# Performance work log

Hardware: AMD Instinct MI355X
Metric: run time of the kernel (lower is better)

The kernel has to match this reference:

```python
import jax, jax.numpy as jnp
import numpy as np

N = 1024      # codeword length (input_size == output_size)
H1 = 3072     # edges of Tanner graph 1
H2 = 4096     # edges of Tanner graph 2
D1 = 6        # per-row mask degree, graph 1
D2 = 8        # per-row mask degree, graph 2
B = 2048      # batch
CLIP = 0.999999


def _row_indices(rng, rows, cols, deg):
    # deg distinct column indices per row (nonzeros of the binary CN mask)
    u = rng.random((rows, cols))
    return np.argsort(u, axis=1)[:, :deg].astype(np.int32)


def setup_inputs() -> dict:
    key = jax.random.key(0)
    ks = jax.random.split(key, 12)
    rng = np.random.default_rng(0)
    x = jax.random.normal(ks[0], (B, N), dtype=jnp.float32) * 2.0
    # CN-update masks as index lists
    idx1_first = jnp.asarray(_row_indices(rng, H1, N, D1))
    idx1_mid = jnp.asarray(_row_indices(rng, H1, H1, D1))
    idx2_first = jnp.asarray(_row_indices(rng, H2, N, D2))
    idx2_mid = jnp.asarray(_row_indices(rng, H2, H2, D2))
    # VN-update weights: xavier-like init pre-multiplied by sparse binary mask
    def sparse_w(k, shape, p):
        k1, k2 = jax.random.split(k)
        w = jax.random.normal(k1, shape, dtype=jnp.float32) * (1.0 / np.sqrt(shape[1]))
        m = (jax.random.uniform(k2, shape) < p).astype(jnp.float32)
        return w * m
    Wv1 = jnp.stack([sparse_w(jax.random.fold_in(ks[1], i), (H1, H1), 0.01) for i in range(5)])
    Wout1 = jnp.stack([sparse_w(jax.random.fold_in(ks[2], i), (N, H1), 0.01) for i in range(5)])
    Wv2 = jnp.stack([sparse_w(jax.random.fold_in(ks[3], i), (H2, H2), 0.01) for i in range(5)])
    Wout2 = jnp.stack([sparse_w(jax.random.fold_in(ks[4], i), (N, H2), 0.01) for i in range(5)])
    # bias scaling vectors: init eye(N) in the torch module; small perturbation to avoid triviality
    S = jnp.stack([jnp.eye(N, dtype=jnp.float32)
                   + 0.01 * jax.random.normal(jax.random.fold_in(ks[5], i), (N, N), dtype=jnp.float32)
                   for i in range(10)])
    B1 = jax.random.normal(ks[6], (N, H1), dtype=jnp.float32) * 0.02
    B2 = jax.random.normal(ks[7], (N, H2), dtype=jnp.float32) * 0.02
    return {"x": x, "S": S, "B1": B1, "B2": B2,
            "Wv1": Wv1, "Wout1": Wout1, "Wv2": Wv2, "Wout2": Wout2,
            "idx1_first": idx1_first, "idx1_mid": idx1_mid,
            "idx2_first": idx2_first, "idx2_mid": idx2_mid}


def cn_update(x, idx):
    # x: (B, in), idx: (out, deg) -> (B, out)
    vals = x[:, idx]                                   # (B, out, deg) gather
    nz = vals != 0.0
    prod = jnp.prod(jnp.where(nz, vals, 1.0), axis=-1)  # zeros act as 1
    return jnp.where(jnp.any(nz, axis=-1), prod, 0.0)   # all-zero rows -> 0


def reference(x, S, B1, B2, Wv1, Wout1, Wv2, Wout2,
              idx1_first, idx1_mid, idx2_first, idx2_mid):
    llrs = []
    for k in range(10):  # 10 unrolled BP iterations, alternating the two graphs
        g1 = (k % 2 == 0)
        j = k // 2
        Bm = B1 if g1 else B2
        Wv = Wv1[j] if g1 else Wv2[j]
        Wo = Wout1[j] if g1 else Wout2[j]
        idf = idx1_first if g1 else idx2_first
        idm = idx1_mid if g1 else idx2_mid
        chS = x @ S[k]                                  # Channel_LLR @ bias_scaling
        t = jnp.tanh(0.5 * x)
        t = jnp.clip(cn_update(t, idf), -CLIP, CLIP)
        t = 2.0 * jnp.arctanh(t)
        t = jnp.tanh(0.5 * (t @ Wv.T + chS @ Bm))
        t = jnp.clip(cn_update(t, idm), -CLIP, CLIP)
        t = 2.0 * jnp.arctanh(t)
        x = t @ Wo.T + chS
        llrs.append(jax.nn.sigmoid(x))
    return tuple(llrs)
```

## Files before the change

kernel.cpp:

```cpp
#include <hip/hip_runtime.h>
#include <hip/hip_bf16.h>
#include <stdint.h>
#include <stddef.h>

using bf16 = __hip_bfloat16;
typedef __attribute__((ext_vector_type(8))) short short8;
typedef __attribute__((ext_vector_type(2))) float f32x2;
typedef __attribute__((ext_vector_type(4))) float f32x4;
typedef __attribute__((ext_vector_type(4))) unsigned u32x4;

constexpr int BATCH = 2048;
constexpr int NN    = 1024;
constexpr int H1C   = 3072;
constexpr int H2C   = 4096;
constexpr int CAP   = 128;

constexpr int ROW_WV1 = 0;
constexpr int ROW_WO1 = 5 * H1C;
constexpr int ROW_WV2 = ROW_WO1 + 5 * NN;
constexpr int ROW_WO2 = ROW_WV2 + 5 * H2C;
constexpr int ROWS_TOTAL = ROW_WO2 + 5 * NN;

__device__ __forceinline__ unsigned short f2bf(float f) {
  unsigned u = __float_as_uint(f);
  unsigned r = 0x7FFFu + ((u >> 16) & 1u);
  return (unsigned short)((u + r) >> 16);
}
__device__ __forceinline__ float bf2f(short s) {
  return __uint_as_float(((unsigned)(unsigned short)s) << 16);
}

__device__ __forceinline__ unsigned short phi_enc(float x) {
  const float e = expf(-fabsf(x));
  const float phi = logf((1.f + e) / (1.f - e));
  return (unsigned short)(f2bf(phi) | (unsigned short)((__float_as_uint(x) >> 31) << 15));
}

__device__ __forceinline__ void gload16(const void* g, void* lds_base) {
  __builtin_amdgcn_global_load_lds(
      (const __attribute__((address_space(1))) void*)g,
      (__attribute__((address_space(3))) void*)lds_base, 16, 0, 0);
}

template<int D>
__device__ __forceinline__ void cn_math(const short8* v, float* rs) {
  float s[8];
  unsigned sg[8];
  bool any[8];
#pragma unroll
  for (int e = 0; e < 8; ++e) { s[e] = 0.f; sg[e] = 0u; any[e] = false; }
#pragma unroll
  for (int d = 0; d < D; ++d) {
#pragma unroll
    for (int e = 0; e < 8; ++e) {
      const unsigned bits = (unsigned)(unsigned short)v[d][e];
      sg[e] ^= bits >> 15;
      const unsigned a = bits & 0x7FFFu;
      const bool nz = (a != 0x7F80u);
      any[e] |= nz;
      s[e] += nz ? __uint_as_float(a << 16) : 0.f;
    }
  }
#pragma unroll
  for (int e = 0; e < 8; ++e) {
    const float y = fmaxf(s[e], 1.0000005e-6f);
    const float u = expf(-y);
    float r = logf((1.f + u) / (1.f - u));
    r = any[e] ? r : 0.f;
    rs[e] = __uint_as_float(__float_as_uint(r) | (sg[e] << 31));
  }
}

__device__ __forceinline__ void cn_store_fp8(const float* rs, uint8_t* dst) {
  int lo = 0, hi = 0;
  lo = __builtin_amdgcn_cvt_pk_fp8_f32(rs[0], rs[1], lo, false);
  lo = __builtin_amdgcn_cvt_pk_fp8_f32(rs[2], rs[3], lo, true);
  hi = __builtin_amdgcn_cvt_pk_fp8_f32(rs[4], rs[5], hi, false);
  hi = __builtin_amdgcn_cvt_pk_fp8_f32(rs[6], rs[7], hi, true);
  int2 o; o.x = lo; o.y = hi;
  *(int2*)dst = o;
}

__global__ __launch_bounds__(256, 2) void gemm_bt(
    const bf16* __restrict__ A, const bf16* __restrict__ BT,
    float* __restrict__ C, bf16* __restrict__ Cb, const float* __restrict__ add,
    int M, int Nd, int K)
{
  __shared__ bf16 As[128 * 32];
  __shared__ bf16 Bs[128 * 32];
  const int tid  = threadIdx.x;
  const int lane = tid & 63;
  const int w    = tid >> 6;
  const int bn = blockIdx.x, bm = blockIdx.y;
  const int wm = (w >> 1) * 64, wn = (w & 1) * 64;
  const int l15 = lane & 15;
  const int lk  = (lane >> 4) * 8;
  const int ld4 = (lane >> 4) * 4;
  const int sr  = lane >> 2;
  const int kc  = (lane & 3) * 8;

  f32x4 acc[4][4];
#pragma unroll
  for (int i = 0; i < 4; ++i)
#pragma unroll
    for (int j = 0; j < 4; ++j)
#pragma unroll
      for (int e = 0; e < 4; ++e) acc[i][j][e] = 0.f;

  const size_t rA = (size_t)bm * 128;
  const size_t rB = (size_t)bn * 128;

  for (int kt = 0; kt < K; kt += 32) {
#pragma unroll
    for (int c = 0; c < 2; ++c) {
      const int slot = w * 2 + c;
      const int r = slot * 16 + sr;
      gload16(A  + (rA + r) * (size_t)K + kt + kc, &As[slot * 512]);
      gload16(BT + (rB + r) * (size_t)K + kt + kc, &Bs[slot * 512]);
    }
    __syncthreads();
    short8 af[4], bfr[4];
#pragma unroll
    for (int f = 0; f < 4; ++f) {
      af[f]  = *(const short8*)&As[(wm + f * 16 + l15) * 32 + lk];
      bfr[f] = *(const short8*)&Bs[(wn + f * 16 + l15) * 32 + lk];
    }
#pragma unroll
    for (int i = 0; i < 4; ++i)
#pragma unroll
      for (int j = 0; j < 4; ++j)
        acc[i][j] = __builtin_amdgcn_mfma_f32_16x16x32_bf16(af[i], bfr[j], acc[i][j], 0, 0, 0);
    __syncthreads();
  }

#pragma unroll
  for (int i = 0; i < 4; ++i) {
    const int row0 = bm * 128 + wm + i * 16 + ld4;
#pragma unroll
    for (int j = 0; j < 4; ++j) {
      const int col = bn * 128 + wn + j * 16 + l15;
#pragma unroll
      for (int e = 0; e < 4; ++e) {
        const size_t o = (size_t)(row0 + e) * Nd + col;
        float v = acc[i][j][e];
        if (add) v += add[o];
        if (C)  C[o] = v;
        if (Cb) Cb[o] = __float2bfloat16(v);
      }
    }
  }
}

template<int D>
__global__ __launch_bounds__(256, 2) void zgemm_cn(
    const bf16* __restrict__ A, const bf16* __restrict__ BT, bf16* __restrict__ Cb,
    int K, int gb,
    const unsigned short* __restrict__ src, const int* __restrict__ idx,
    uint8_t* __restrict__ outf8)
{
  __shared__ bf16 As[128 * 32];
  __shared__ bf16 Bs[128 * 32];
  const int bid = blockIdx.x;
  if (bid < gb) {
    const int tid  = threadIdx.x;
    const int lane = tid & 63;
    const int w    = tid >> 6;
    const int bn = bid & 15;
    const int bm = bid >> 4;
    const int wm = (w >> 1) * 64, wn = (w & 1) * 64;
    const int l15 = lane & 15;
    const int lk  = (lane >> 4) * 8;
    const int ld4 = (lane >> 4) * 4;
    const int sr  = lane >> 2;
    const int kc  = (lane & 3) * 8;

    f32x4 acc[4][4];
#pragma unroll
    for (int i = 0; i < 4; ++i)
#pragma unroll
      for (int j = 0; j < 4; ++j)
#pragma unroll
        for (int e = 0; e < 4; ++e) acc[i][j][e] = 0.f;

    const size_t rA = (size_t)bm * 128;
    const size_t rB = (size_t)bn * 128;

    for (int kt = 0; kt < K; kt += 32) {
#pragma unroll
      for (int c = 0; c < 2; ++c) {
        const int slot = w * 2 + c;
        const int r = slot * 16 + sr;
        gload16(A  + (rA + r) * (size_t)K + kt + kc, &As[slot * 512]);
        gload16(BT + (rB + r) * (size_t)K + kt + kc, &Bs[slot * 512]);
      }
      __syncthreads();
      short8 af[4], bfr[4];
#pragma unroll
      for (int f = 0; f < 4; ++f) {
        af[f]  = *(const short8*)&As[(wm + f * 16 + l15) * 32 + lk];
        bfr[f] = *(const short8*)&Bs[(wn + f * 16 + l15) * 32 + lk];
      }
#pragma unroll
      for (int i = 0; i < 4; ++i)
#pragma unroll
        for (int j = 0; j < 4; ++j)
          acc[i][j] = __builtin_amdgcn_mfma_f32_16x16x32_bf16(af[i], bfr[j], acc[i][j], 0, 0, 0);
      __syncthreads();
    }

#pragma unroll
    for (int i = 0; i < 4; ++i) {
      const int row0 = bm * 128 + wm + i * 16 + ld4;
#pragma unroll
      for (int j = 0; j < 4; ++j) {
        const int col = bn * 128 + wn + j * 16 + l15;
#pragma unroll
        for (int e = 0; e < 4; ++e)
          Cb[(size_t)(row0 + e) * BATCH + col] = __float2bfloat16(acc[i][j][e]);
      }
    }
  } else {
    const int h = bid - gb;
    const int b = threadIdx.x * 8;
    const int* ir = idx + (size_t)h * D;
    int rows[D];
#pragma unroll
    for (int d = 0; d < D; ++d) rows[d] = ir[d];
    short8 v[D];
#pragma unroll
    for (int d = 0; d < D; ++d)
      v[d] = *(const short8*)(src + (size_t)rows[d] * BATCH + b);
    float rs[8];
    cn_math<D>(v, rs);
    cn_store_fp8(rs, outf8 + (size_t)h * BATCH + b);
  }
}

__global__ __launch_bounds__(256) void prep_smit(const float* __restrict__ S, bf16* __restrict__ out)
{
  __shared__ float ls[64][65];
  const int k = blockIdx.z;
  const int n0 = blockIdx.x * 64, m0 = blockIdx.y * 64;
  const float* Sk = S + (size_t)k * NN * NN;
  bf16* ok = out + (size_t)k * NN * NN;
  const int tc = threadIdx.x & 63, tr = threadIdx.x >> 6;
#pragma unroll
  for (int i = 0; i < 16; ++i) {
    const int r = tr + i * 4;
    ls[r][tc] = Sk[(size_t)(m0 + r) * NN + n0 + tc];
  }
  __syncthreads();
#pragma unroll
  for (int i = 0; i < 16; ++i) {
    const int r = tr + i * 4;
    float v = ls[tc][r] - ((m0 + tc) == (n0 + r) ? 1.f : 0.f);
    ok[(size_t)(n0 + r) * NN + m0 + tc] = __float2bfloat16(v);
  }
}

__global__ __launch_bounds__(256) void prep_bt(const float* __restrict__ Bsrc, bf16* __restrict__ out, int H)
{
  __shared__ float ls[64][65];
  const int h0 = blockIdx.x * 64, n0 = blockIdx.y * 64;
  const int tc = threadIdx.x & 63, tr = threadIdx.x >> 6;
#pragma unroll
  for (int i = 0; i < 16; ++i) {
    const int r = tr + i * 4;
    ls[r][tc] = Bsrc[(size_t)(n0 + r) * H + h0 + tc];
  }
  __syncthreads();
#pragma unroll
  for (int i = 0; i < 16; ++i) {
    const int r = tr + i * 4;
    out[(size_t)(h0 + r) * NN + n0 + tc] = __float2bfloat16(ls[tc][r]);
  }
}

__global__ __launch_bounds__(256) void csr_build(
    const float* __restrict__ W, int rowlen,
    unsigned* __restrict__ pack, int* __restrict__ nnz, int row_off)
{
  const int row = blockIdx.x;
  const float* wr = W + (size_t)row * rowlen;
  const size_t base = (size_t)(row_off + row) * CAP;
  __shared__ int wtot[4];
  __shared__ int cbase;
  if (threadIdx.x == 0) cbase = 0;
  __syncthreads();
  const int lane = threadIdx.x & 63, wv = threadIdx.x >> 6;
  for (int c0 = 0; c0 < rowlen; c0 += 256) {
    const int c = c0 + threadIdx.x;
    const float v = wr[c];
    const bool nz = (v != 0.f);
    const unsigned long long m = __ballot(nz);
    const int rank = __popcll(m & ((1ull << lane) - 1ull));
    if (lane == 0) wtot[wv] = __popcll(m);
    __syncthreads();
    int pre = cbase;
    for (int i = 0; i < wv; ++i) pre += wtot[i];
    if (nz) {
      const int p = pre + rank;
      if (p < CAP) pack[base + p] = ((unsigned)f2bf(v) << 16) | (unsigned)c;
    }
    __syncthreads();
    if (threadIdx.x == 0) cbase += wtot[0] + wtot[1] + wtot[2] + wtot[3];
    __syncthreads();
  }
  if (threadIdx.x == 0) nnz[row_off + row] = (cbase < CAP ? cbase : CAP);
}

template<int D>
__global__ __launch_bounds__(256) void cn_kernel(
    const unsigned short* __restrict__ src,
    const int* __restrict__ idx,
    uint8_t* __restrict__ out)
{
  const int h = blockIdx.x;
  const int b = threadIdx.x * 8;
  const int* ir = idx + (size_t)h * D;
  int rows[D];
#pragma unroll
  for (int d = 0; d < D; ++d) rows[d] = ir[d];
  short8 v[D];
#pragma unroll
  for (int d = 0; d < D; ++d)
    v[d] = *(const short8*)(src + (size_t)rows[d] * BATCH + b);
  float rs[8];
  cn_math<D>(v, rs);
  cn_store_fp8(rs, out + (size_t)h * BATCH + b);
}

__global__ __launch_bounds__(256) void sparse_wv(
    const unsigned short* __restrict__ zb, const uint8_t* __restrict__ t1f8,
    const unsigned* __restrict__ pack, const int* __restrict__ nnz,
    int rowoff, unsigned short* __restrict__ t2p)
{
  const int h = blockIdx.x;
  const int b = threadIdx.x * 8;
  const int rg = rowoff + h;
  const unsigned* pr = pack + (size_t)rg * CAP;
  const int n = nnz[rg];
  const short8 z = *(const short8*)(zb + (size_t)h * BATCH + b);
  f32x4 a0, a1;
#pragma unroll
  for (int e = 0; e < 4; ++e) { a0[e] = bf2f(z[e]); a1[e] = bf2f(z[e + 4]); }
  int j = 0;
  for (; j + 4 <= n; j += 4) {
    const u32x4 w4 = *(const u32x4*)(pr + j);
    int2 t[4];
#pragma unroll
    for (int q = 0; q < 4; ++q)
      t[q] = *(const int2*)(t1f8 + (size_t)(w4[q] & 0xFFFFu) * BATCH + b);
#pragma unroll
    for (int q = 0; q < 4; ++q) {
      const float v = bf2f((short)(w4[q] >> 16));
      const f32x2 p01 = __builtin_amdgcn_cvt_pk_f32_fp8(t[q].x, false);
      const f32x2 p23 = __builtin_amdgcn_cvt_pk_f32_fp8(t[q].x, true);
      const f32x2 p45 = __builtin_amdgcn_cvt_pk_f32_fp8(t[q].y, false);
      const f32x2 p67 = __builtin_amdgcn_cvt_pk_f32_fp8(t[q].y, true);
      a0[0] += v * p01[0]; a0[1] += v * p01[1];
      a0[2] += v * p23[0]; a0[3] += v * p23[1];
      a1[0] += v * p45[0]; a1[1] += v * p45[1];
      a1[2] += v * p67[0]; a1[3] += v * p67[1];
    }
  }
  for (; j < n; ++j) {
    const unsigned pk = pr[j];
    const float v = bf2f((short)(pk >> 16));
    const int2 t = *(const int2*)(t1f8 + (size_t)(pk & 0xFFFFu) * BATCH + b);
    const f32x2 p01 = __builtin_amdgcn_cvt_pk_f32_fp8(t.x, false);
    const f32x2 p23 = __builtin_amdgcn_cvt_pk_f32_fp8(t.x, true);
    const f32x2 p45 = __builtin_amdgcn_cvt_pk_f32_fp8(t.y, false);
    const f32x2 p67 = __builtin_amdgcn_cvt_pk_f32_fp8(t.y, true);
    a0[0] += v * p01[0]; a0[1] += v * p01[1];
    a0[2] += v * p23[0]; a0[3] += v * p23[1];
    a1[0] += v * p45[0]; a1[1] += v * p45[1];
    a1[2] += v * p67[0]; a1[3] += v * p67[1];
  }
  short8 ov;
#pragma unroll
  for (int e = 0; e < 4; ++e) {
    ov[e]     = (short)phi_enc(a0[e]);
    ov[e + 4] = (short)phi_enc(a1[e]);
  }
  *(short8*)(t2p + (size_t)h * BATCH + b) = ov;
}

__global__ __launch_bounds__(256) void sparse_wo(
    const uint8_t* __restrict__ t3f8,
    const unsigned* __restrict__ pack, const int* __restrict__ nnz,
    int rowoff, float* __restrict__ xp)
{
  const int nrow = blockIdx.x;
  const int b = threadIdx.x * 8;
  const int rg = rowoff + nrow;
  const unsigned* pr = pack + (size_t)rg * CAP;
  const int cnt = nnz[rg];
  f32x4 a0 = {0.f, 0.f, 0.f, 0.f};
  f32x4 a1 = {0.f, 0.f, 0.f, 0.f};
  int j = 0;
  for (; j + 4 <= cnt; j += 4) {
    const u32x4 w4 = *(const u32x4*)(pr + j);
    int2 t[4];
#pragma unroll
    for (int q = 0; q < 4; ++q)
      t[q] = *(const int2*)(t3f8 + (size_t)(w4[q] & 0xFFFFu) * BATCH + b);
#pragma unroll
    for (int q = 0; q < 4; ++q) {
      const float v = bf2f((short)(w4[q] >> 16));
      const f32x2 p01 = __builtin_amdgcn_cvt_pk_f32_fp8(t[q].x, false);
      const f32x2 p23 = __builtin_amdgcn_cvt_pk_f32_fp8(t[q].x, true);
      const f32x2 p45 = __builtin_amdgcn_cvt_pk_f32_fp8(t[q].y, false);
      const f32x2 p67 = __builtin_amdgcn_cvt_pk_f32_fp8(t[q].y, true);
      a0[0] += v * p01[0]; a0[1] += v * p01[1];
      a0[2] += v * p23[0]; a0[3] += v * p23[1];
      a1[0] += v * p45[0]; a1[1] += v * p45[1];
      a1[2] += v * p67[0]; a1[3] += v * p67[1];
    }
  }
  for (; j < cnt; ++j) {
    const unsigned pk = pr[j];
    const float v = bf2f((short)(pk >> 16));
    const int2 t = *(const int2*)(t3f8 + (size_t)(pk & 0xFFFFu) * BATCH + b);
    const f32x2 p01 = __builtin_amdgcn_cvt_pk_f32_fp8(t.x, false);
    const f32x2 p23 = __builtin_amdgcn_cvt_pk_f32_fp8(t.x, true);
    const f32x2 p45 = __builtin_amdgcn_cvt_pk_f32_fp8(t.y, false);
    const f32x2 p67 = __builtin_amdgcn_cvt_pk_f32_fp8(t.y, true);
    a0[0] += v * p01[0]; a0[1] += v * p01[1];
    a0[2] += v * p23[0]; a0[3] += v * p23[1];
    a1[0] += v * p45[0]; a1[1] += v * p45[1];
    a1[2] += v * p67[0]; a1[3] += v * p67[1];
  }
  float* orow = xp + (size_t)nrow * BATCH + b;
  *(f32x4*)orow = a0;
  *(f32x4*)(orow + 4) = a1;
}

__global__ __launch_bounds__(256) void fuse_out(
    const float* __restrict__ xpT,
    const float* __restrict__ chS,
    float* __restrict__ dout,
    float* __restrict__ xf,
    bf16* __restrict__ xb,
    unsigned short* __restrict__ tfT)
{
  __shared__ float lc[64][65];
  __shared__ float lx[64][65];
  const int n0 = blockIdx.x * 64, b0 = blockIdx.y * 64;
  const int tc = threadIdx.x & 63, tr = threadIdx.x >> 6;
#pragma unroll
  for (int i = 0; i < 16; ++i) {
    const int r = tr + i * 4;
    lc[r][tc] = chS[(size_t)(b0 + r) * NN + n0 + tc];
    lx[r][tc] = xpT[(size_t)(n0 + r) * BATCH + b0 + tc];
  }
  __syncthreads();
#pragma unroll
  for (int i = 0; i < 16; ++i) {
    const int r = tr + i * 4;
    const float v = lc[r][tc] + lx[tc][r];
    const size_t o = (size_t)(b0 + r) * NN + n0 + tc;
    dout[o] = 1.f / (1.f + expf(-v));
    xf[o] = v;
    xb[o] = __float2bfloat16(v);
  }
#pragma unroll
  for (int i = 0; i < 16; ++i) {
    const int r = tr + i * 4;
    const float v = lc[tc][r] + lx[r][tc];
    tfT[(size_t)(n0 + r) * BATCH + b0 + tc] = phi_enc(v);
  }
}

__global__ __launch_bounds__(256) void init_prep(
    const float* __restrict__ x, bf16* __restrict__ xb, unsigned short* __restrict__ tfT)
{
  __shared__ float ls[64][65];
  const int n0 = blockIdx.x * 64, b0 = blockIdx.y * 64;
  const int tc = threadIdx.x & 63, tr = threadIdx.x >> 6;
#pragma unroll
  for (int i = 0; i < 16; ++i) {
    const int r = tr + i * 4;
    const size_t o = (size_t)(b0 + r) * NN + n0 + tc;
    const float v = x[o];
    ls[r][tc] = v;
    xb[o] = __float2bfloat16(v);
  }
  __syncthreads();
#pragma unroll
  for (int i = 0; i < 16; ++i) {
    const int r = tr + i * 4;
    tfT[(size_t)(n0 + r) * BATCH + b0 + tc] = phi_enc(ls[tc][r]);
  }
}

extern "C" void kernel_launch(void* const* d_in, const int* in_sizes, int n_in,
                              void* d_out, int out_size, void* d_ws, size_t ws_size,
                              hipStream_t stream)
{
  const float* x_in  = (const float*)d_in[0];
  const float* S     = (const float*)d_in[1];
  const float* B1    = (const float*)d_in[2];
  const float* B2    = (const float*)d_in[3];
  const float* Wv1   = (const float*)d_in[4];
  const float* Wout1 = (const float*)d_in[5];
  const float* Wv2   = (const float*)d_in[6];
  const float* Wout2 = (const float*)d_in[7];
  const int* idx1f   = (const int*)d_in[8];
  const int* idx1m   = (const int*)d_in[9];
  const int* idx2f   = (const int*)d_in[10];
  const int* idx2m   = (const int*)d_in[11];
  float* out = (float*)d_out;

  uint8_t* p = (uint8_t*)d_ws;
  auto alloc = [&](size_t bytes) -> void* {
    void* r = p;
    p += (bytes + 255) & ~(size_t)255;
    return r;
  };
  bf16*  SmIT = (bf16*)alloc((size_t)10 * NN * NN * sizeof(bf16));
  bf16*  B1T  = (bf16*)alloc((size_t)H1C * NN * sizeof(bf16));
  bf16*  B2T  = (bf16*)alloc((size_t)H2C * NN * sizeof(bf16));
  unsigned* cpack = (unsigned*)alloc((size_t)ROWS_TOTAL * CAP * sizeof(unsigned));
  int*   cnnz  = (int*)alloc((size_t)ROWS_TOTAL * sizeof(int));
  float* xf   = (float*)alloc((size_t)BATCH * NN * sizeof(float));
  bf16*  xb   = (bf16*)alloc((size_t)BATCH * NN * sizeof(bf16));
  unsigned short* tfT = (unsigned short*)alloc((size_t)NN * BATCH * sizeof(unsigned short));
  float* chS  = (float*)alloc((size_t)BATCH * NN * sizeof(float));
  bf16*  chSb = (bf16*)alloc((size_t)BATCH * NN * sizeof(bf16));
  uint8_t* t1f8 = (uint8_t*)alloc((size_t)H2C * BATCH);
  uint8_t* t3f8 = (uint8_t*)alloc((size_t)H2C * BATCH);
  unsigned short* zTb = (unsigned short*)alloc((size_t)H2C * BATCH * sizeof(unsigned short));
  unsigned short* t2p = (unsigned short*)alloc((size_t)H2C * BATCH * sizeof(unsigned short));
  float* xpT  = (float*)alloc((size_t)NN * BATCH * sizeof(float));
  (void)ws_size; (void)in_sizes; (void)n_in; (void)out_size;

  prep_smit<<<dim3(NN / 64, NN / 64, 10), 256, 0, stream>>>(S, SmIT);
  prep_bt<<<dim3(H1C / 64, NN / 64), 256, 0, stream>>>(B1, B1T, H1C);
  prep_bt<<<dim3(H2C / 64, NN / 64), 256, 0, stream>>>(B2, B2T, H2C);
  csr_build<<<5 * H1C, 256, 0, stream>>>(Wv1,   H1C, cpack, cnnz, ROW_WV1);
  csr_build<<<5 * NN,  256, 0, stream>>>(Wout1, H1C, cpack, cnnz, ROW_WO1);
  csr_build<<<5 * H2C, 256, 0, stream>>>(Wv2,   H2C, cpack, cnnz, ROW_WV2);
  csr_build<<<5 * NN,  256, 0, stream>>>(Wout2, H2C, cpack, cnnz, ROW_WO2);
  init_prep<<<dim3(NN / 64, BATCH / 64), 256, 0, stream>>>(x_in, xb, tfT);

  for (int k = 0; k < 10; ++k) {
    const bool g1 = (k % 2 == 0);
    const int j = k / 2;
    const int H = g1 ? H1C : H2C;
    const bf16* BmT = g1 ? B1T : B2T;
    const int* idf = g1 ? idx1f : idx2f;
    const int* idm = g1 ? idx1m : idx2m;
    const int wv_off = g1 ? (ROW_WV1 + j * H1C) : (ROW_WV2 + j * H2C);
    const int wo_off = g1 ? (ROW_WO1 + j * NN)  : (ROW_WO2 + j * NN);
    const float* xcur = (k == 0) ? x_in : xf;
    const int gb = (BATCH / 128) * (H / 128);

    gemm_bt<<<dim3(NN / 128, BATCH / 128), 256, 0, stream>>>(
        xb, SmIT + (size_t)k * NN * NN, chS, chSb, xcur, BATCH, NN, NN);
    if (g1) zgemm_cn<6><<<gb + H, 256, 0, stream>>>(BmT, chSb, (bf16*)zTb, NN, gb, tfT, idf, t1f8);
    else    zgemm_cn<8><<<gb + H, 256, 0, stream>>>(BmT, chSb, (bf16*)zTb, NN, gb, tfT, idf, t1f8);
    sparse_wv<<<dim3(H, 1), 256, 0, stream>>>(zTb, t1f8, cpack, cnnz, wv_off, t2p);
    if (g1) cn_kernel<6><<<dim3(H, 1), 256, 0, stream>>>(t2p, idm, t3f8);
    else    cn_kernel<8><<<dim3(H, 1), 256, 0, stream>>>(t2p, idm, t3f8);
    sparse_wo<<<dim3(NN, 1), 256, 0, stream>>>(t3f8, cpack, cnnz, wo_off, xpT);
    fuse_out<<<dim3(NN / 64, BATCH / 64), 256, 0, stream>>>(
        xpT, chS, out + (size_t)k * BATCH * NN, xf, xb, tfT);
  }
}
```

Before: 1.816 ms.

## Re-pair independent stages into shared launches: chS GEMM with first CN, Z GEMM with Wv SpMM

The schedule now runs the first check-node gather in the same launch as the channel-scaling GEMM, which no longer uses a 128x128 tile but a 64x128 one to get more blocks. The Wv sparse product runs in the same launch as the dense bias GEMM, writing a separate buffer, and a new small kernel adds the two and applies phi. The aim is to fill the GPU with independent work and drop a serial dependency per iteration. The cost is an extra elementwise pass and buffer per iteration. csr_build is also vectorised to four floats per thread.

```diff
diff --git a/kernel.cpp b/kernel.cpp
--- a/kernel.cpp
+++ b/kernel.cpp
@@ -14,6 +14,7 @@
 constexpr int H1C   = 3072;
 constexpr int H2C   = 4096;
 constexpr int CAP   = 128;
+constexpr int CHS_GB = (NN / 128) * (BATCH / 64);
 
 constexpr int ROW_WV1 = 0;
 constexpr int ROW_WO1 = 5 * H1C;
@@ -81,82 +82,106 @@
   *(int2*)dst = o;
 }
 
-__global__ __launch_bounds__(256, 2) void gemm_bt(
+template<int D>
+__global__ __launch_bounds__(256, 2) void chs_cn(
     const bf16* __restrict__ A, const bf16* __restrict__ BT,
     float* __restrict__ C, bf16* __restrict__ Cb, const float* __restrict__ add,
-    int M, int Nd, int K)
-{
-  __shared__ bf16 As[128 * 32];
+    const unsigned short* __restrict__ src, const int* __restrict__ idx,
+    uint8_t* __restrict__ outf8)
+{
+  __shared__ bf16 As[64 * 32];
   __shared__ bf16 Bs[128 * 32];
-  const int tid  = threadIdx.x;
-  const int lane = tid & 63;
-  const int w    = tid >> 6;
-  const int bn = blockIdx.x, bm = blockIdx.y;
-  const int wm = (w >> 1) * 64, wn = (w & 1) * 64;
-  const int l15 = lane & 15;
-  const int lk  = (lane >> 4) * 8;
-  const int ld4 = (lane >> 4) * 4;
-  const int sr  = lane >> 2;
-  const int kc  = (lane & 3) * 8;
-
-  f32x4 acc[4][4];
-#pragma unroll
-  for (int i = 0; i < 4; ++i)
-#pragma unroll
-    for (int j = 0; j < 4; ++j)
-#pragma unroll
-      for (int e = 0; e < 4; ++e) acc[i][j][e] = 0.f;
-
-  const size_t rA = (size_t)bm * 128;
-  const size_t rB = (size_t)bn * 128;
-
-  for (int kt = 0; kt < K; kt += 32) {
-#pragma unroll
-    for (int c = 0; c < 2; ++c) {
-      const int slot = w * 2 + c;
-      const int r = slot * 16 + sr;
-      gload16(A  + (rA + r) * (size_t)K + kt + kc, &As[slot * 512]);
-      gload16(BT + (rB + r) * (size_t)K + kt + kc, &Bs[slot * 512]);
-    }
-    __syncthreads();
-    short8 af[4], bfr[4];
-#pragma unroll
-    for (int f = 0; f < 4; ++f) {
-      af[f]  = *(const short8*)&As[(wm + f * 16 + l15) * 32 + lk];
-      bfr[f] = *(const short8*)&Bs[(wn + f * 16 + l15) * 32 + lk];
-    }
+  const int bid = blockIdx.x;
+  const int tid = threadIdx.x;
+  if (bid < CHS_GB) {
+    const int lane = tid & 63;
+    const int w    = tid >> 6;
+    const int bn = bid & 7;
+    const int bm = bid >> 3;
+    const int wn = w * 32;
+    const int l15 = lane & 15;
+    const int lk  = (lane >> 4) * 8;
+    const int ld4 = (lane >> 4) * 4;
+    const int sr  = lane >> 2;
+    const int kc  = (lane & 3) * 8;
+
+    f32x4 acc[4][2];
 #pragma unroll
     for (int i = 0; i < 4; ++i)
 #pragma unroll
-      for (int j = 0; j < 4; ++j)
-        acc[i][j] = __builtin_amdgcn_mfma_f32_16x16x32_bf16(af[i], bfr[j], acc[i][j], 0, 0, 0);
-    __syncthreads();
-  }
-
-#pragma unroll
-  for (int i = 0; i < 4; ++i) {
-    const int row0 = bm * 128 + wm + i * 16 + ld4;
-#pragma unroll
-    for (int j = 0; j < 4; ++j) {
-      const int col = bn * 128 + wn + j * 16 + l15;
-#pragma unroll
-      for (int e = 0; e < 4; ++e) {
-        const size_t o = (size_t)(row0 + e) * Nd + col;
-        float v = acc[i][j][e];
-        if (add) v += add[o];
-        if (C)  C[o] = v;
-        if (Cb) Cb[o] = __float2bfloat16(v);
+      for (int j = 0; j < 2; ++j)
+#pragma unroll
+        for (int e = 0; e < 4; ++e) acc[i][j][e] = 0.f;
+
+    const size_t rA = (size_t)bm * 64;
+    const size_t rB = (size_t)bn * 128;
+
+    for (int kt = 0; kt < NN; kt += 32) {
+#pragma unroll
+      for (int c = 0; c < 3; ++c) {
+        const int slot = w * 3 + c;
+        if (slot < 4) {
+          const int r = slot * 16 + sr;
+          gload16(A + (rA + r) * (size_t)NN + kt + kc, &As[slot * 512]);
+        } else {
+          const int r = (slot - 4) * 16 + sr;
+          gload16(BT + (rB + r) * (size_t)NN + kt + kc, &Bs[(slot - 4) * 512]);
+        }
       }
-    }
-  }
-}
-
-template<int D>
-__global__ __launch_bounds__(256, 2) void zgemm_cn(
+      __syncthreads();
+      short8 af[4], bfr[2];
+#pragma unroll
+      for (int f = 0; f < 4; ++f)
+        af[f] = *(const short8*)&As[(f * 16 + l15) * 32 + lk];
+#pragma unroll
+      for (int f = 0; f < 2; ++f)
+        bfr[f] = *(const short8*)&Bs[(wn + f * 16 + l15) * 32 + lk];
+#pragma unroll
+      for (int i = 0; i < 4; ++i)
+#pragma unroll
+        for (int j = 0; j < 2; ++j)
+          acc[i][j] = __builtin_amdgcn_mfma_f32_16x16x32_bf16(af[i], bfr[j], acc[i][j], 0, 0, 0);
+      __syncthreads();
+    }
+
+#pragma unroll
+    for (int i = 0; i < 4; ++i) {
+      const int row0 = bm * 64 + i * 16 + ld4;
+#pragma unroll
+      for (int j = 0; j < 2; ++j) {
+        const int col = bn * 128 + wn + j * 16 + l15;
+#pragma unroll
+        for (int e = 0; e < 4; ++e) {
+          const size_t o = (size_t)(row0 + e) * NN + col;
+          float v = acc[i][j][e] + add[o];
+          C[o] = v;
+          Cb[o] = __float2bfloat16(v);
+        }
+      }
+    }
+  } else {
+    const int h = bid - CHS_GB;
+    const int b = tid * 8;
+    const int* ir = idx + (size_t)h * D;
+    int rows[D];
+#pragma unroll
+    for (int d = 0; d < D; ++d) rows[d] = ir[d];
+    short8 v[D];
+#pragma unroll
+    for (int d = 0; d < D; ++d)
+      v[d] = *(const short8*)(src + (size_t)rows[d] * BATCH + b);
+    float rs[8];
+    cn_math<D>(v, rs);
+    cn_store_fp8(rs, outf8 + (size_t)h * BATCH + b);
+  }
+}
+
+__global__ __launch_bounds__(256, 2) void zgemm_wv(
     const bf16* __restrict__ A, const bf16* __restrict__ BT, bf16* __restrict__ Cb,
     int K, int gb,
-    const unsigned short* __restrict__ src, const int* __restrict__ idx,
-    uint8_t* __restrict__ outf8)
+    const uint8_t* __restrict__ t1f8,
+    const unsigned* __restrict__ pack, const int* __restrict__ nnz,
+    int rowoff, unsigned short* __restrict__ gTb)
 {
   __shared__ bf16 As[128 * 32];
   __shared__ bf16 Bs[128 * 32];
@@ -222,18 +247,67 @@
   } else {
     const int h = bid - gb;
     const int b = threadIdx.x * 8;
-    const int* ir = idx + (size_t)h * D;
-    int rows[D];
-#pragma unroll
-    for (int d = 0; d < D; ++d) rows[d] = ir[d];
-    short8 v[D];
-#pragma unroll
-    for (int d = 0; d < D; ++d)
-      v[d] = *(const short8*)(src + (size_t)rows[d] * BATCH + b);
-    float rs[8];
-    cn_math<D>(v, rs);
-    cn_store_fp8(rs, outf8 + (size_t)h * BATCH + b);
-  }
+    const int rg = rowoff + h;
+    const unsigned* pr = pack + (size_t)rg * CAP;
+    const int n = nnz[rg];
+    f32x4 a0 = {0.f, 0.f, 0.f, 0.f};
+    f32x4 a1 = {0.f, 0.f, 0.f, 0.f};
+    int j = 0;
+    for (; j + 4 <= n; j += 4) {
+      const u32x4 w4 = *(const u32x4*)(pr + j);
+      int2 t[4];
+#pragma unroll
+      for (int q = 0; q < 4; ++q)
+        t[q] = *(const int2*)(t1f8 + (size_t)(w4[q] & 0xFFFFu) * BATCH + b);
+#pragma unroll
+      for (int q = 0; q < 4; ++q) {
+        const float v = bf2f((short)(w4[q] >> 16));
+        const f32x2 p01 = __builtin_amdgcn_cvt_pk_f32_fp8(t[q].x, false);
+        const f32x2 p23 = __builtin_amdgcn_cvt_pk_f32_fp8(t[q].x, true);
+        const f32x2 p45 = __builtin_amdgcn_cvt_pk_f32_fp8(t[q].y, false);
+        const f32x2 p67 = __builtin_amdgcn_cvt_pk_f32_fp8(t[q].y, true);
+        a0[0] += v * p01[0]; a0[1] += v * p01[1];
+        a0[2] += v * p23[0]; a0[3] += v * p23[1];
+        a1[0] += v * p45[0]; a1[1] += v * p45[1];
+        a1[2] += v * p67[0]; a1[3] += v * p67[1];
+      }
+    }
+    for (; j < n; ++j) {
+      const unsigned pk = pr[j];
+      const float v = bf2f((short)(pk >> 16));
+      const int2 t = *(const int2*)(t1f8 + (size_t)(pk & 0xFFFFu) * BATCH + b);
+      const f32x2 p01 = __builtin_amdgcn_cvt_pk_f32_fp8(t.x, false);
+      const f32x2 p23 = __builtin_amdgcn_cvt_pk_f32_fp8(t.x, true);
+      const f32x2 p45 = __builtin_amdgcn_cvt_pk_f32_fp8(t.y, false);
+      const f32x2 p67 = __builtin_amdgcn_cvt_pk_f32_fp8(t.y, true);
+      a0[0] += v * p01[0]; a0[1] += v * p01[1];
+      a0[2] += v * p23[0]; a0[3] += v * p23[1];
+      a1[0] += v * p45[0]; a1[1] += v * p45[1];
+      a1[2] += v * p67[0]; a1[3] += v * p67[1];
+    }
+    short8 ov;
+#pragma unroll
+    for (int e = 0; e < 4; ++e) {
+      ov[e]     = (short)f2bf(a0[e]);
+      ov[e + 4] = (short)f2bf(a1[e]);
+    }
+    *(short8*)(gTb + (size_t)h * BATCH + b) = ov;
+  }
+}
+
+__global__ __launch_bounds__(256) void phi_add(
+    const unsigned short* __restrict__ zb, const unsigned short* __restrict__ gbuf,
+    unsigned short* __restrict__ t2p)
+{
+  const int h = blockIdx.x;
+  const int b = threadIdx.x * 8;
+  const short8 z = *(const short8*)(zb + (size_t)h * BATCH + b);
+  const short8 g = *(const short8*)(gbuf + (size_t)h * BATCH + b);
+  short8 ov;
+#pragma unroll
+  for (int e = 0; e < 8; ++e)
+    ov[e] = (short)phi_enc(bf2f(z[e]) + bf2f(g[e]));
+  *(short8*)(t2p + (size_t)h * BATCH + b) = ov;
 }
 
 __global__ __launch_bounds__(256) void prep_smit(const float* __restrict__ S, bf16* __restrict__ out)
@@ -288,19 +362,29 @@
   if (threadIdx.x == 0) cbase = 0;
   __syncthreads();
   const int lane = threadIdx.x & 63, wv = threadIdx.x >> 6;
-  for (int c0 = 0; c0 < rowlen; c0 += 256) {
-    const int c = c0 + threadIdx.x;
-    const float v = wr[c];
-    const bool nz = (v != 0.f);
-    const unsigned long long m = __ballot(nz);
-    const int rank = __popcll(m & ((1ull << lane) - 1ull));
-    if (lane == 0) wtot[wv] = __popcll(m);
+  const unsigned long long lanemask = (1ull << lane) - 1ull;
+  for (int c0 = 0; c0 < rowlen; c0 += 1024) {
+    const int c = c0 + threadIdx.x * 4;
+    const f32x4 v = *(const f32x4*)(wr + c);
+    unsigned long long m[4];
+#pragma unroll
+    for (int e = 0; e < 4; ++e) m[e] = __ballot(v[e] != 0.f);
+    int pre_lane = 0;
+#pragma unroll
+    for (int e = 0; e < 4; ++e) pre_lane += __popcll(m[e] & lanemask);
+    if (lane == 0)
+      wtot[wv] = __popcll(m[0]) + __popcll(m[1]) + __popcll(m[2]) + __popcll(m[3]);
     __syncthreads();
-    int pre = cbase;
+    int pre = cbase + pre_lane;
     for (int i = 0; i < wv; ++i) pre += wtot[i];
-    if (nz) {
-      const int p = pre + rank;
-      if (p < CAP) pack[base + p] = ((unsigned)f2bf(v) << 16) | (unsigned)c;
+    int off = 0;
+#pragma unroll
+    for (int e = 0; e < 4; ++e) {
+      if (v[e] != 0.f) {
+        const int p = pre + off;
+        if (p < CAP) pack[base + p] = ((unsigned)f2bf(v[e]) << 16) | (unsigned)(c + e);
+        ++off;
+      }
     }
     __syncthreads();
     if (threadIdx.x == 0) cbase += wtot[0] + wtot[1] + wtot[2] + wtot[3];
@@ -328,62 +412,6 @@
   float rs[8];
   cn_math<D>(v, rs);
   cn_store_fp8(rs, out + (size_t)h * BATCH + b);
-}
-
-__global__ __launch_bounds__(256) void sparse_wv(
-    const unsigned short* __restrict__ zb, const uint8_t* __restrict__ t1f8,
-    const unsigned* __restrict__ pack, const int* __restrict__ nnz,
-    int rowoff, unsigned short* __restrict__ t2p)
-{
-  const int h = blockIdx.x;
-  const int b = threadIdx.x * 8;
-  const int rg = rowoff + h;
-  const unsigned* pr = pack + (size_t)rg * CAP;
-  const int n = nnz[rg];
-  const short8 z = *(const short8*)(zb + (size_t)h * BATCH + b);
-  f32x4 a0, a1;
-#pragma unroll
-  for (int e = 0; e < 4; ++e) { a0[e] = bf2f(z[e]); a1[e] = bf2f(z[e + 4]); }
-  int j = 0;
-  for (; j + 4 <= n; j += 4) {
-    const u32x4 w4 = *(const u32x4*)(pr + j);
-    int2 t[4];
-#pragma unroll
-    for (int q = 0; q < 4; ++q)
-      t[q] = *(const int2*)(t1f8 + (size_t)(w4[q] & 0xFFFFu) * BATCH + b);
-#pragma unroll
-    for (int q = 0; q < 4; ++q) {
-      const float v = bf2f((short)(w4[q] >> 16));
-      const f32x2 p01 = __builtin_amdgcn_cvt_pk_f32_fp8(t[q].x, false);
-      const f32x2 p23 = __builtin_amdgcn_cvt_pk_f32_fp8(t[q].x, true);
-      const f32x2 p45 = __builtin_amdgcn_cvt_pk_f32_fp8(t[q].y, false);
-      const f32x2 p67 = __builtin_amdgcn_cvt_pk_f32_fp8(t[q].y, true);
-      a0[0] += v * p01[0]; a0[1] += v * p01[1];
-      a0[2] += v * p23[0]; a0[3] += v * p23[1];
-      a1[0] += v * p45[0]; a1[1] += v * p45[1];
-      a1[2] += v * p67[0]; a1[3] += v * p67[1];
-    }
-  }
-  for (; j < n; ++j) {
-    const unsigned pk = pr[j];
-    const float v = bf2f((short)(pk >> 16));
-    const int2 t = *(const int2*)(t1f8 + (size_t)(pk & 0xFFFFu) * BATCH + b);
-    const f32x2 p01 = __builtin_amdgcn_cvt_pk_f32_fp8(t.x, false);
-    const f32x2 p23 = __builtin_amdgcn_cvt_pk_f32_fp8(t.x, true);
-    const f32x2 p45 = __builtin_amdgcn_cvt_pk_f32_fp8(t.y, false);
-    const f32x2 p67 = __builtin_amdgcn_cvt_pk_f32_fp8(t.y, true);
-    a0[0] += v * p01[0]; a0[1] += v * p01[1];
-    a0[2] += v * p23[0]; a0[3] += v * p23[1];
-    a1[0] += v * p45[0]; a1[1] += v * p45[1];
-    a1[2] += v * p67[0]; a1[3] += v * p67[1];
-  }
-  short8 ov;
-#pragma unroll
-  for (int e = 0; e < 4; ++e) {
-    ov[e]     = (short)phi_enc(a0[e]);
-    ov[e + 4] = (short)phi_enc(a1[e]);
-  }
-  *(short8*)(t2p + (size_t)h * BATCH + b) = ov;
 }
 
 __global__ __launch_bounds__(256) void sparse_wo(
@@ -531,6 +559,7 @@
   uint8_t* t1f8 = (uint8_t*)alloc((size_t)H2C * BATCH);
   uint8_t* t3f8 = (uint8_t*)alloc((size_t)H2C * BATCH);
   unsigned short* zTb = (unsigned short*)alloc((size_t)H2C * BATCH * sizeof(unsigned short));
+  unsigned short* gTb = (unsigned short*)alloc((size_t)H2C * BATCH * sizeof(unsigned short));
   unsigned short* t2p = (unsigned short*)alloc((size_t)H2C * BATCH * sizeof(unsigned short));
   float* xpT  = (float*)alloc((size_t)NN * BATCH * sizeof(float));
   (void)ws_size; (void)in_sizes; (void)n_in; (void)out_size;
@@ -556,11 +585,13 @@
     const float* xcur = (k == 0) ? x_in : xf;
     const int gb = (BATCH / 128) * (H / 128);
 
-    gemm_bt<<<dim3(NN / 128, BATCH / 128), 256, 0, stream>>>(
-        xb, SmIT + (size_t)k * NN * NN, chS, chSb, xcur, BATCH, NN, NN);
-    if (g1) zgemm_cn<6><<<gb + H, 256, 0, stream>>>(BmT, chSb, (bf16*)zTb, NN, gb, tfT, idf, t1f8);
-    else    zgemm_cn<8><<<gb + H, 256, 0, stream>>>(BmT, chSb, (bf16*)zTb, NN, gb, tfT, idf, t1f8);
-    sparse_wv<<<dim3(H, 1), 256, 0, stream>>>(zTb, t1f8, cpack, cnnz, wv_off, t2p);
+    if (g1) chs_cn<6><<<CHS_GB + H, 256, 0, stream>>>(
+        xb, SmIT + (size_t)k * NN * NN, chS, chSb, xcur, tfT, idf, t1f8);
+    else    chs_cn<8><<<CHS_GB + H, 256, 0, stream>>>(
+        xb, SmIT + (size_t)k * NN * NN, chS, chSb, xcur, tfT, idf, t1f8);
+    zgemm_wv<<<gb + H, 256, 0, stream>>>(
+        BmT, chSb, (bf16*)zTb, NN, gb, t1f8, cpack, cnnz, wv_off, gTb);
+    phi_add<<<H, 256, 0, stream>>>(zTb, gTb, t2p);
     if (g1) cn_kernel<6><<<dim3(H, 1), 256, 0, stream>>>(t2p, idm, t3f8);
     else    cn_kernel<8><<<dim3(H, 1), 256, 0, stream>>>(t2p, idm, t3f8);
     sparse_wo<<<dim3(NN, 1), 256, 0, stream>>>(t3f8, cpack, cnnz, wo_off, xpT);
```

New measurement: 1.487 ms. 18.1% less time.
